# Optimization experiments

Hardware: AMD Instinct MI355X
Metric: run time of the kernel (lower is better)

Reference implementation:

```python
import jax, jax.numpy as jnp
import numpy as np

T = 100000
H = 74          # input_size == hidden_size == 74
L = 3           # lstm_layers
OUT = 1


def setup_inputs() -> dict:
    key = jax.random.key(0)
    ks = jax.random.split(key, 8)
    s = 1.0 / np.sqrt(H)  # PyTorch LSTM/Linear init scale
    seasons = jax.random.normal(ks[0], (T, H), dtype=jnp.float32)
    # PyTorch gate order: i, f, g, o -> stacked as [L, 4H, H]
    W_ih = jax.random.uniform(ks[1], (L, 4 * H, H), jnp.float32, -s, s)
    W_hh = jax.random.uniform(ks[2], (L, 4 * H, H), jnp.float32, -s, s)
    b_ih = jax.random.uniform(ks[3], (L, 4 * H), jnp.float32, -s, s)
    b_hh = jax.random.uniform(ks[4], (L, 4 * H), jnp.float32, -s, s)
    W_lin = jax.random.uniform(ks[5], (OUT, H), jnp.float32, -s, s)
    b_lin = jax.random.uniform(ks[6], (OUT,), jnp.float32, -s, s)
    return {"seasons": seasons, "W_ih": W_ih, "W_hh": W_hh,
            "b_ih": b_ih, "b_hh": b_hh, "W_lin": W_lin, "b_lin": b_lin}


def _lstm_step(h, c, x, W_ih, W_hh, b_ih, b_hh):
    # h, c: [L, H]; x: [H]. Sequential over layers (L=3, structurally distinct state).
    new_h, new_c = [], []
    inp = x
    for l in range(L):
        gates = W_ih[l] @ inp + b_ih[l] + W_hh[l] @ h[l] + b_hh[l]  # [4H]
        i, f, g, o = jnp.split(gates, 4)
        i = jax.nn.sigmoid(i)
        f = jax.nn.sigmoid(f)
        g = jnp.tanh(g)
        o = jax.nn.sigmoid(o)
        cl = f * c[l] + i * g
        hl = o * jnp.tanh(cl)
        new_h.append(hl)
        new_c.append(cl)
        inp = hl
    return jnp.stack(new_h), jnp.stack(new_c), inp


def reference(seasons, W_ih, W_hh, b_ih, b_hh, W_lin, b_lin):
    def step(carry, x):
        h, c = carry
        h, c, top = _lstm_step(h, c, x, W_ih, W_hh, b_ih, b_hh)
        pred = jax.nn.relu(W_lin @ top + b_lin)  # [1]
        return (h, c), pred

    init = (jnp.zeros((L, H), jnp.float32), jnp.zeros((L, H), jnp.float32))
    _, preds = jax.lax.scan(step, init, seasons)  # [T, 1]
    # original cats [1,1,1] tensors along dim 0 -> [T, 1, 1]
    return preds.reshape(T, 1, 1)
```

## Files before the change

kernel.cpp:

```cpp
#include <hip/hip_runtime.h>
#include <math.h>

#define TT    100000
#define HH    74
#define G4    296
#define KH    40
#define SLOT  80
#define ZSLOT 304
#define NT    768
#define W5    640
#define W6    704

typedef float f4 __attribute__((ext_vector_type(4)));

#define ALD(p)    __hip_atomic_load((p),  __ATOMIC_RELAXED, __HIP_MEMORY_SCOPE_AGENT)
#define ALDA(p)   __hip_atomic_load((p),  __ATOMIC_ACQUIRE, __HIP_MEMORY_SCOPE_AGENT)
#define AST(p,v)  __hip_atomic_store((p),(v),__ATOMIC_RELAXED, __HIP_MEMORY_SCOPE_AGENT)
#define ASTR(p,v) __hip_atomic_store((p),(v),__ATOMIC_RELEASE, __HIP_MEMORY_SCOPE_AGENT)

#define BAR() asm volatile("s_waitcnt lgkmcnt(0)\n\ts_barrier" ::: "memory")

__global__ void init_ctrl(unsigned* ctrl) {
    ctrl[threadIdx.x] = 0u;
}

__launch_bounds__(NT, 1)
__global__ void lstm_pipe6(const float* __restrict__ seasons,
                           const float* __restrict__ W_ih,
                           const float* __restrict__ W_hh,
                           const float* __restrict__ b_ih,
                           const float* __restrict__ b_hh,
                           const float* __restrict__ W_lin,
                           const float* __restrict__ b_lin,
                           float* __restrict__ out,
                           unsigned* ctrl,
                           float* zbase, float* hbase, int CZ, int CH)
{
    const int  bid = blockIdx.x;
    const int  l   = bid >> 1;
    const bool isA = (bid & 1) == 0;
    const int  tid = threadIdx.x;

    __shared__ __align__(16) float sIn[2][SLOT];
    __shared__ __align__(16) float sZ[2][ZSLOT];
    __shared__ __align__(16) float sH[SLOT];
    __shared__ float sG[G4];

    unsigned* cnt_out = ctrl + bid * 32;
    unsigned* cnt_in  = ctrl + (bid > 0 ? (bid - 1) * 32 : 0);
    unsigned* cnt_dn  = ctrl + (bid < 5 ? (bid + 1) * 32 : 0);

    float* zring     = zbase + (size_t)l * CZ * ZSLOT;
    float* hring_out = hbase + (size_t)l * CH * SLOT;
    float* hring_in  = (l > 0) ? hbase + (size_t)(l-1) * CH * SLOT : (float*)0;

    if (tid < SLOT) sH[tid] = 0.0f;
    if (tid >= SLOT && tid < SLOT + 2*(SLOT-HH)) {
        int k = tid - SLOT;
        sIn[k/(SLOT-HH)][HH + k%(SLOT-HH)] = 0.0f;
    }

    const bool isRowT = (tid < W5);
    const int  row  = (tid >> 6) * 32 + ((tid & 63) >> 1);
    const int  half = tid & 1;
    const int  wrow = (row < G4) ? row : (G4 - 1);

    f4 w0={0,0,0,0},w1={0,0,0,0},w2={0,0,0,0},w3={0,0,0,0},w4={0,0,0,0},
       w5={0,0,0,0},w6={0,0,0,0},w7={0,0,0,0},w8={0,0,0,0},w9={0,0,0,0};
    float bias = 0.0f;

    if (isRowT) {
        const bool  isG = (wrow >= 2*HH) && (wrow < 3*HH);
        const float sc  = isG ? 2.0f : 1.0f;
        const float* src = (isA ? W_ih : W_hh) + (size_t)(l*G4 + wrow) * HH;
#define LDW(V, Q) { \
        int k0 = half*KH + 4*(Q); \
        int ka=k0, kb=k0+1, kc=k0+2, kd=k0+3; \
        float va=src[ka<HH?ka:0], vb=src[kb<HH?kb:0]; \
        float vc=src[kc<HH?kc:0], vd=src[kd<HH?kd:0]; \
        V[0] = ka<HH ? sc*va : 0.0f;  V[1] = kb<HH ? sc*vb : 0.0f; \
        V[2] = kc<HH ? sc*vc : 0.0f;  V[3] = kd<HH ? sc*vd : 0.0f; }
        LDW(w0,0) LDW(w1,1) LDW(w2,2) LDW(w3,3) LDW(w4,4)
        LDW(w5,5) LDW(w6,6) LDW(w7,7) LDW(w8,8) LDW(w9,9)
#undef LDW
        asm volatile("" : "+v"(w0),"+v"(w1),"+v"(w2),"+v"(w3),"+v"(w4),
                          "+v"(w5),"+v"(w6),"+v"(w7),"+v"(w8),"+v"(w9));
        if (isA && half == 0)
            bias = sc * (b_ih[l*G4 + wrow] + b_hh[l*G4 + wrow]);
    }

    float wl0 = 0.f, wl1 = 0.f, blin = 0.f;
    if (bid == 5 && tid >= W6) {
        int lane = tid - W6;
        wl0 = W_lin[lane];
        wl1 = (lane < HH-64) ? W_lin[64 + lane] : 0.0f;
        blin = b_lin[0];
    }

    __syncthreads();

    float irA0=0.f, irA1=0.f, irB0=0.f, irB1=0.f;
    float zA0=0.f,zA1=0.f,zA2=0.f,zA3=0.f,zA4=0.f;
    float zB0=0.f,zB1=0.f,zB2=0.f,zB3=0.f,zB4=0.f;
    unsigned cin = 0, cons = 0;
    if (tid >= W5 && tid < W6) {
        const int lane = tid - W5;
        if (isA) {
            if (l == 0) {
                sIn[0][lane] = seasons[lane];
                if (lane < HH-64) sIn[0][64+lane] = seasons[64+lane];
                irA0 = seasons[HH + lane];
                if (lane < HH-64) irA1 = seasons[HH + 64 + lane];
                irB0 = seasons[2*HH + lane];
                if (lane < HH-64) irB1 = seasons[2*HH + 64 + lane];
            } else {
                do { cin = ALDA(cnt_in); } while (cin < 3u);
                sIn[0][lane] = ALD(hring_in + lane);
                if (lane < HH-64) sIn[0][64+lane] = ALD(hring_in + 64 + lane);
                const float* r1 = hring_in + (size_t)(1 % CH) * SLOT;
                irA0 = ALD(r1 + lane);
                if (lane < HH-64) irA1 = ALD(r1 + 64 + lane);
                const float* r2 = hring_in + (size_t)(2 % CH) * SLOT;
                irB0 = ALD(r2 + lane);
                if (lane < HH-64) irB1 = ALD(r2 + 64 + lane);
            }
        } else {
            do { cin = ALDA(cnt_in); } while (cin < 3u);
            sZ[0][lane]       = ALD(zring + lane);
            sZ[0][64 + lane]  = ALD(zring + 64 + lane);
            sZ[0][128 + lane] = ALD(zring + 128 + lane);
            sZ[0][192 + lane] = ALD(zring + 192 + lane);
            if (lane < G4-256) sZ[0][256 + lane] = ALD(zring + 256 + lane);
            const float* r1 = zring + (size_t)(1 % CZ) * ZSLOT;
            zA0 = ALD(r1 + lane);        zA1 = ALD(r1 + 64 + lane);
            zA2 = ALD(r1 + 128 + lane);  zA3 = ALD(r1 + 192 + lane);
            zA4 = (lane < G4-256) ? ALD(r1 + 256 + lane) : 0.0f;
            const float* r2 = zring + (size_t)(2 % CZ) * ZSLOT;
            zB0 = ALD(r2 + lane);        zB1 = ALD(r2 + 64 + lane);
            zB2 = ALD(r2 + 128 + lane);  zB3 = ALD(r2 + 192 + lane);
            zB4 = (lane < G4-256) ? ALD(r2 + 256 + lane) : 0.0f;
        }
    }
    __syncthreads();

    float c = 0.0f;

#define ACC4(W, Q) { f4 v_ = vv[Q]; \
            a0 = fmaf(W[0], v_[0], a0); a1 = fmaf(W[1], v_[1], a1); \
            a2 = fmaf(W[2], v_[2], a2); a3 = fmaf(W[3], v_[3], a3); }

#define STEP(T, IR0, IR1, Z0, Z1, Z2, Z3, Z4)                                   \
{                                                                               \
    const int b_ = (T) & 1;                                                     \
    if (isRowT) {                                                               \
        float a0, a1 = 0.f, a2 = 0.f, a3 = 0.f;                                 \
        const f4* vv;                                                           \
        if (isA) { vv = ((const f4*)sIn[b_]) + half*(KH/4); a0 = bias; }        \
        else { vv = ((const f4*)sH) + half*(KH/4);                              \
               a0 = (half == 0 && row < G4) ? sZ[b_][row] : 0.0f; }             \
        ACC4(w0,0) ACC4(w1,1) ACC4(w2,2) ACC4(w3,3) ACC4(w4,4)                  \
        ACC4(w5,5) ACC4(w6,6) ACC4(w7,7) ACC4(w8,8) ACC4(w9,9)                  \
        float p_ = (a0 + a1) + (a2 + a3);                                       \
        p_ += __shfl_xor(p_, 1, 64);                                            \
        if (isA) { if (half == 0 && row < G4) sZ[b_][row] = p_; }               \
        else { float s_ = __builtin_amdgcn_rcpf(1.0f + __expf(-p_));            \
               const bool isG_ = (row >= 2*HH) && (row < 3*HH);                 \
               float g_ = isG_ ? fmaf(2.0f, s_, -1.0f) : s_;                    \
               if (half == 0 && row < G4) sG[row] = g_; }                       \
    } else if (tid < W6) {          \
        const int lane = tid - W5;                                              \
        const int nb_ = ((T) + 1) & 1;                                          \
        int s_ = (T) + 3; if (s_ > TT-1) s_ = TT-1;                             \
        if (isA) {                                                              \
            sIn[nb_][lane] = IR0;                                               \
            if (lane < HH-64) sIn[nb_][64+lane] = IR1;                          \
            if (l == 0) {                                                       \
                const float* xs_ = seasons + (size_t)s_ * HH;                   \
                IR0 = xs_[lane];                                                \
                if (lane < HH-64) IR1 = xs_[64+lane];                           \
            } else {                                                            \
                unsigned need_ = (unsigned)(s_ + 1); if (need_ > TT) need_ = TT;\
                if (cin < need_) { do { cin = ALDA(cnt_in); } while (cin < need_); } \
                const float* rs_ = hring_in + (size_t)(s_ % CH) * SLOT;         \
                IR0 = ALD(rs_ + lane);                                          \
                if (lane < HH-64) IR1 = ALD(rs_ + 64 + lane);                   \
                cin = ALD(cnt_in);                                              \
            }                                                                   \
        } else {                                                                \
            sZ[nb_][lane] = Z0; sZ[nb_][64+lane] = Z1;                          \
            sZ[nb_][128+lane] = Z2; sZ[nb_][192+lane] = Z3;                     \
            if (lane < G4-256) sZ[nb_][256+lane] = Z4;                          \
            unsigned need_ = (unsigned)(s_ + 1); if (need_ > TT) need_ = TT;    \
            if (cin < need_) { do { cin = ALDA(cnt_in); } while (cin < need_); }\
            const float* rs_ = zring + (size_t)(s_ % CZ) * ZSLOT;               \
            Z0 = ALD(rs_ + lane); Z1 = ALD(rs_ + 64 + lane);                    \
            Z2 = ALD(rs_ + 128 + lane); Z3 = ALD(rs_ + 192 + lane);             \
            if (lane < G4-256) Z4 = ALD(rs_ + 256 + lane);                      \
            cin = ALD(cnt_in);                                                  \
        }                                                                       \
    } else {                           \
        const int lane = tid - W6;                                              \
        if ((T) > 0) {                                                          \
            if (isA) {                                                          \
                while ((long)((T)-1) - (long)cons > (long)(CZ - 8))             \
                    cons = ALD(cnt_dn);                                         \
                const int ob_ = ((T)-1) & 1;                                    \
                float v0_ = sZ[ob_][lane],      v1_ = sZ[ob_][64+lane];         \
                float v2_ = sZ[ob_][128+lane],  v3_ = sZ[ob_][192+lane];        \
                float v4_ = (lane < G4-256) ? sZ[ob_][256+lane] : 0.0f;         \
                float* rp_ = zring + (size_t)(((T)-1) % CZ) * ZSLOT;            \
                AST(rp_ + lane, v0_);        AST(rp_ + 64 + lane, v1_);         \
                AST(rp_ + 128 + lane, v2_);  AST(rp_ + 192 + lane, v3_);        \
                if (lane < G4-256) AST(rp_ + 256 + lane, v4_);                  \
                if (lane == 0) ASTR(cnt_out, (unsigned)(T));                    \
            } else if (l < 2) {                                                 \
                while ((long)((T)-1) - (long)cons > (long)(CH - 8))             \
                    cons = ALD(cnt_dn);                                         \
                float h0_ = sH[lane];                                           \
                float h1_ = (lane < HH-64) ? sH[64+lane] : 0.0f;                \
                float* rp_ = hring_out + (size_t)(((T)-1) % CH) * SLOT;         \
                AST(rp_ + lane, h0_);                                           \
                if (lane < HH-64) AST(rp_ + 64 + lane, h1_);                    \
                if (lane == 0) ASTR(cnt_out, (unsigned)(T));                    \
            } else {                                                            \
                if (lane == 0) AST(cnt_out, (unsigned)(T));                     \
                float p_ = wl0 * sH[lane];                                      \
                if (lane < HH-64) p_ += wl1 * sH[64 + lane];                    \
                _Pragma("unroll")                                               \
                for (int m_ = 32; m_ >= 1; m_ >>= 1)                            \
                    p_ += __shfl_xor(p_, m_, 64);                               \
                if (lane == 0) out[(T)-1] = fmaxf(p_ + blin, 0.0f);             \
            }                                                                   \
        }                                                                       \
    }                                                                           \
    BAR();                                                                      \
    if (!isA) {                                                                 \
        if (tid < HH) {                                                         \
            float iv_ = sG[tid], fv_ = sG[HH+tid];                              \
            float gv_ = sG[2*HH+tid], ov_ = sG[3*HH+tid];                       \
            c = fmaf(fv_, c, iv_ * gv_);                                        \
            float e_  = __expf(-2.0f * fabsf(c));                               \
            float th_ = copysignf((1.0f - e_) * __builtin_amdgcn_rcpf(1.0f + e_), c); \
            sH[tid] = ov_ * th_;                                                \
        }                                                                       \
        BAR();                                                                  \
    }                                                                           \
}

    for (int t = 0; t < TT; t += 2) {
        STEP(t,     irA0, irA1, zA0, zA1, zA2, zA3, zA4)
        STEP(t + 1, irB0, irB1, zB0, zB1, zB2, zB3, zB4)
    }
#undef STEP
#undef ACC4

    if (tid >= W6) {
        const int lane = tid - W6;
        if (isA) {
            const int ob = (TT-1) & 1;
            float v0 = sZ[ob][lane],      v1 = sZ[ob][64+lane];
            float v2 = sZ[ob][128+lane],  v3 = sZ[ob][192+lane];
            float v4 = (lane < G4-256) ? sZ[ob][256+lane] : 0.0f;
            float* rp = zring + (size_t)((TT-1) % CZ) * ZSLOT;
            AST(rp + lane, v0);        AST(rp + 64 + lane, v1);
            AST(rp + 128 + lane, v2);  AST(rp + 192 + lane, v3);
            if (lane < G4-256) AST(rp + 256 + lane, v4);
            if (lane == 0) ASTR(cnt_out, (unsigned)TT);
        } else if (l < 2) {
            float h0 = sH[lane];
            float h1 = (lane < HH-64) ? sH[64+lane] : 0.0f;
            float* rp = hring_out + (size_t)((TT-1) % CH) * SLOT;
            AST(rp + lane, h0);
            if (lane < HH-64) AST(rp + 64 + lane, h1);
            if (lane == 0) ASTR(cnt_out, (unsigned)TT);
        } else {
            float p = wl0 * sH[lane];
            if (lane < HH-64) p += wl1 * sH[64 + lane];
            #pragma unroll
            for (int m = 32; m >= 1; m >>= 1)
                p += __shfl_xor(p, m, 64);
            if (lane == 0) out[TT-1] = fmaxf(p + blin, 0.0f);
        }
    }
}

extern "C" void kernel_launch(void* const* d_in, const int* in_sizes, int n_in,
                              void* d_out, int out_size, void* d_ws, size_t ws_size,
                              hipStream_t stream)
{
    (void)in_sizes; (void)n_in; (void)out_size;
    const float* seasons = (const float*)d_in[0];
    const float* W_ih  = (const float*)d_in[1];
    const float* W_hh  = (const float*)d_in[2];
    const float* b_ih  = (const float*)d_in[3];
    const float* b_hh  = (const float*)d_in[4];
    const float* W_lin = (const float*)d_in[5];
    const float* b_lin = (const float*)d_in[6];
    float* out = (float*)d_out;

    unsigned* ctrl = (unsigned*)d_ws;
    float* zbase = (float*)((char*)d_ws + 4096);
    long avail = ((long)ws_size - 4096) / 4;
    int CZ = 256, CH = 1024;
    while ((3L*CZ*ZSLOT + 2L*CH*SLOT) > avail && CZ > 16) { CZ >>= 1; CH >>= 1; }
    if (CZ < 16) CZ = 16;
    if (CH < 16) CH = 16;
    float* hbase = zbase + 3L * CZ * ZSLOT;

    hipLaunchKernelGGL(init_ctrl, dim3(1), dim3(256), 0, stream, ctrl);
    hipLaunchKernelGGL(lstm_pipe6, dim3(6), dim3(NT), 0, stream,
                       seasons, W_ih, W_hh, b_ih, b_hh, W_lin, b_lin,
                       out, ctrl, zbase, hbase, CZ, CH);
}
```

Measured before the change: 77.22 ms.

## Remap gate matvec to 4-thread groups of 5 rows, halve block size

Each block now uses 384 threads instead of 768. Groups of 4 threads each compute 5 gate rows over a 20-wide K slice, holding 25 float4 weight registers per thread, and reduce with xor shuffles across the group. The publisher wave now also does the cell/hidden update, and progress counters are released one step earlier, before the data stores. The aim is fewer waves per block barrier and less synchronisation latency on the sequential per-timestep critical path. The cost is higher register pressure and a longer serial FMA chain per thread.

After: 103.0 ms. 33.3% more time.

```diff
diff --git a/kernel.cpp b/kernel.cpp
--- a/kernel.cpp
+++ b/kernel.cpp
@@ -4,12 +4,14 @@
 #define TT    100000
 #define HH    74
 #define G4    296
-#define KH    40
+#define KP    80
+#define QW    20
+#define NGRP  60
 #define SLOT  80
 #define ZSLOT 304
-#define NT    768
-#define W5    640
-#define W6    704
+#define NT    384
+#define WPRE  256
+#define WPUB  320
 
 typedef float f4 __attribute__((ext_vector_type(4)));
 
@@ -24,7 +26,7 @@
     ctrl[threadIdx.x] = 0u;
 }
 
-__launch_bounds__(NT, 1)
+__launch_bounds__(NT, 2)
 __global__ void lstm_pipe6(const float* __restrict__ seasons,
                            const float* __restrict__ W_ih,
                            const float* __restrict__ W_hh,
@@ -44,7 +46,7 @@
     __shared__ __align__(16) float sIn[2][SLOT];
     __shared__ __align__(16) float sZ[2][ZSLOT];
     __shared__ __align__(16) float sH[SLOT];
-    __shared__ float sG[G4];
+    __shared__ float sG[ZSLOT];
 
     unsigned* cnt_out = ctrl + bid * 32;
     unsigned* cnt_in  = ctrl + (bid > 0 ? (bid - 1) * 32 : 0);
@@ -54,44 +56,58 @@
     float* hring_out = hbase + (size_t)l * CH * SLOT;
     float* hring_in  = (l > 0) ? hbase + (size_t)(l-1) * CH * SLOT : (float*)0;
 
-    if (tid < SLOT) sH[tid] = 0.0f;
-    if (tid >= SLOT && tid < SLOT + 2*(SLOT-HH)) {
-        int k = tid - SLOT;
-        sIn[k/(SLOT-HH)][HH + k%(SLOT-HH)] = 0.0f;
-    }
-
-    const bool isRowT = (tid < W5);
-    const int  row  = (tid >> 6) * 32 + ((tid & 63) >> 1);
-    const int  half = tid & 1;
-    const int  wrow = (row < G4) ? row : (G4 - 1);
-
-    f4 w0={0,0,0,0},w1={0,0,0,0},w2={0,0,0,0},w3={0,0,0,0},w4={0,0,0,0},
-       w5={0,0,0,0},w6={0,0,0,0},w7={0,0,0,0},w8={0,0,0,0},w9={0,0,0,0};
-    float bias = 0.0f;
+    if (tid < SLOT) { sH[tid] = 0.0f; sIn[0][tid] = 0.0f; sIn[1][tid] = 0.0f; }
+
+    const bool isRowT = (tid < WPRE);
+    const int  g  = tid >> 2;
+    const int  q  = tid & 3;
+    const int  gg = (g < NGRP) ? g : NGRP - 1;
+
+#define DW(n) f4 n = {0.f,0.f,0.f,0.f}
+    DW(w00);DW(w01);DW(w02);DW(w03);DW(w04); DW(w10);DW(w11);DW(w12);DW(w13);DW(w14);
+    DW(w20);DW(w21);DW(w22);DW(w23);DW(w24); DW(w30);DW(w31);DW(w32);DW(w33);DW(w34);
+    DW(w40);DW(w41);DW(w42);DW(w43);DW(w44);
+#undef DW
+    float biasA = 0.f, biasB = 0.f;
 
     if (isRowT) {
-        const bool  isG = (wrow >= 2*HH) && (wrow < 3*HH);
-        const float sc  = isG ? 2.0f : 1.0f;
-        const float* src = (isA ? W_ih : W_hh) + (size_t)(l*G4 + wrow) * HH;
-#define LDW(V, Q) { \
-        int k0 = half*KH + 4*(Q); \
-        int ka=k0, kb=k0+1, kc=k0+2, kd=k0+3; \
-        float va=src[ka<HH?ka:0], vb=src[kb<HH?kb:0]; \
-        float vc=src[kc<HH?kc:0], vd=src[kd<HH?kd:0]; \
-        V[0] = ka<HH ? sc*va : 0.0f;  V[1] = kb<HH ? sc*vb : 0.0f; \
-        V[2] = kc<HH ? sc*vc : 0.0f;  V[3] = kd<HH ? sc*vd : 0.0f; }
-        LDW(w0,0) LDW(w1,1) LDW(w2,2) LDW(w3,3) LDW(w4,4)
-        LDW(w5,5) LDW(w6,6) LDW(w7,7) LDW(w8,8) LDW(w9,9)
+        const float* Wm = (isA ? W_ih : W_hh) + (size_t)l * G4 * HH;
+#define LDW(V, I, S) { \
+        int r_ = 5*gg + (I); if (r_ > G4-1) r_ = G4-1; \
+        float sc_ = (r_ >= 2*HH && r_ < 3*HH) ? 2.0f : 1.0f;   \
+        const float* p_ = Wm + (size_t)r_ * HH; \
+        int k0_ = QW*q + 4*(S); \
+        int ka_ = k0_;   if (ka_ > HH-1) ka_ = HH-1;    \
+        int kb_ = k0_+1; if (kb_ > HH-1) kb_ = HH-1;    \
+        int kc_ = k0_+2; if (kc_ > HH-1) kc_ = HH-1; \
+        int kd_ = k0_+3; if (kd_ > HH-1) kd_ = HH-1; \
+        V[0] = sc_*p_[ka_]; V[1] = sc_*p_[kb_]; V[2] = sc_*p_[kc_]; V[3] = sc_*p_[kd_]; }
+        LDW(w00,0,0) LDW(w01,0,1) LDW(w02,0,2) LDW(w03,0,3) LDW(w04,0,4)
+        LDW(w10,1,0) LDW(w11,1,1) LDW(w12,1,2) LDW(w13,1,3) LDW(w14,1,4)
+        LDW(w20,2,0) LDW(w21,2,1) LDW(w22,2,2) LDW(w23,2,3) LDW(w24,2,4)
+        LDW(w30,3,0) LDW(w31,3,1) LDW(w32,3,2) LDW(w33,3,3) LDW(w34,3,4)
+        LDW(w40,4,0) LDW(w41,4,1) LDW(w42,4,2) LDW(w43,4,3) LDW(w44,4,4)
 #undef LDW
-        asm volatile("" : "+v"(w0),"+v"(w1),"+v"(w2),"+v"(w3),"+v"(w4),
-                          "+v"(w5),"+v"(w6),"+v"(w7),"+v"(w8),"+v"(w9));
-        if (isA && half == 0)
-            bias = sc * (b_ih[l*G4 + wrow] + b_hh[l*G4 + wrow]);
+        asm volatile("" : "+v"(w00),"+v"(w01),"+v"(w02),"+v"(w03),"+v"(w04),
+                          "+v"(w10),"+v"(w11),"+v"(w12),"+v"(w13),"+v"(w14),
+                          "+v"(w20),"+v"(w21),"+v"(w22),"+v"(w23),"+v"(w24));
+        asm volatile("" : "+v"(w30),"+v"(w31),"+v"(w32),"+v"(w33),"+v"(w34),
+                          "+v"(w40),"+v"(w41),"+v"(w42),"+v"(w43),"+v"(w44));
+        if (isA) {
+            int r0 = 5*gg + q; if (r0 > G4-1) r0 = G4-1;
+            float s0 = (r0 >= 2*HH && r0 < 3*HH) ? 2.0f : 1.0f;
+            biasA = s0 * (b_ih[l*G4 + r0] + b_hh[l*G4 + r0]);
+            if (q == 3) {
+                int r4 = 5*gg + 4; if (r4 > G4-1) r4 = G4-1;
+                float s4 = (r4 >= 2*HH && r4 < 3*HH) ? 2.0f : 1.0f;
+                biasB = s4 * (b_ih[l*G4 + r4] + b_hh[l*G4 + r4]);
+            }
+        }
     }
 
     float wl0 = 0.f, wl1 = 0.f, blin = 0.f;
-    if (bid == 5 && tid >= W6) {
-        int lane = tid - W6;
+    if (bid == 5 && tid >= WPUB) {
+        int lane = tid - WPUB;
         wl0 = W_lin[lane];
         wl1 = (lane < HH-64) ? W_lin[64 + lane] : 0.0f;
         blin = b_lin[0];
@@ -103,8 +119,8 @@
     float zA0=0.f,zA1=0.f,zA2=0.f,zA3=0.f,zA4=0.f;
     float zB0=0.f,zB1=0.f,zB2=0.f,zB3=0.f,zB4=0.f;
     unsigned cin = 0, cons = 0;
-    if (tid >= W5 && tid < W6) {
-        const int lane = tid - W5;
+    if (tid >= WPRE && tid < WPUB) {
+        const int lane = tid - WPRE;
         if (isA) {
             if (l == 0) {
                 sIn[0][lane] = seasons[lane];
@@ -143,108 +159,128 @@
     }
     __syncthreads();
 
-    float c = 0.0f;
-
-#define ACC4(W, Q) { f4 v_ = vv[Q]; \
-            a0 = fmaf(W[0], v_[0], a0); a1 = fmaf(W[1], v_[1], a1); \
-            a2 = fmaf(W[2], v_[2], a2); a3 = fmaf(W[3], v_[3], a3); }
-
-#define STEP(T, IR0, IR1, Z0, Z1, Z2, Z3, Z4)                                   \
-{                                                                               \
-    const int b_ = (T) & 1;                                                     \
-    if (isRowT) {                                                               \
-        float a0, a1 = 0.f, a2 = 0.f, a3 = 0.f;                                 \
-        const f4* vv;                                                           \
-        if (isA) { vv = ((const f4*)sIn[b_]) + half*(KH/4); a0 = bias; }        \
-        else { vv = ((const f4*)sH) + half*(KH/4);                              \
-               a0 = (half == 0 && row < G4) ? sZ[b_][row] : 0.0f; }             \
-        ACC4(w0,0) ACC4(w1,1) ACC4(w2,2) ACC4(w3,3) ACC4(w4,4)                  \
-        ACC4(w5,5) ACC4(w6,6) ACC4(w7,7) ACC4(w8,8) ACC4(w9,9)                  \
-        float p_ = (a0 + a1) + (a2 + a3);                                       \
-        p_ += __shfl_xor(p_, 1, 64);                                            \
-        if (isA) { if (half == 0 && row < G4) sZ[b_][row] = p_; }               \
-        else { float s_ = __builtin_amdgcn_rcpf(1.0f + __expf(-p_));            \
-               const bool isG_ = (row >= 2*HH) && (row < 3*HH);                 \
-               float g_ = isG_ ? fmaf(2.0f, s_, -1.0f) : s_;                    \
-               if (half == 0 && row < G4) sG[row] = g_; }                       \
-    } else if (tid < W6) {          \
-        const int lane = tid - W5;                                              \
-        const int nb_ = ((T) + 1) & 1;                                          \
-        int s_ = (T) + 3; if (s_ > TT-1) s_ = TT-1;                             \
-        if (isA) {                                                              \
-            sIn[nb_][lane] = IR0;                                               \
-            if (lane < HH-64) sIn[nb_][64+lane] = IR1;                          \
-            if (l == 0) {                                                       \
-                const float* xs_ = seasons + (size_t)s_ * HH;                   \
-                IR0 = xs_[lane];                                                \
-                if (lane < HH-64) IR1 = xs_[64+lane];                           \
-            } else {                                                            \
-                unsigned need_ = (unsigned)(s_ + 1); if (need_ > TT) need_ = TT;\
+    float c0 = 0.0f, c1 = 0.0f;
+
+#define ACC(A_, W_, V_) A_ = fmaf(W_[0],V_[0], fmaf(W_[1],V_[1], fmaf(W_[2],V_[2], fmaf(W_[3],V_[3], A_))))
+
+#define STEP(T, IR0, IR1, Z0, Z1, Z2, Z3, Z4)                                     \
+{                                                                                 \
+    const int b_ = (T) & 1;                                                       \
+    if (isRowT) {                                                                 \
+        const f4* vv = ((const f4*)(isA ? sIn[b_] : sH)) + q*(QW/4);              \
+        f4 v0=vv[0], v1=vv[1], v2=vv[2], v3=vv[3], v4=vv[4];                      \
+        float a0=0.f,a1=0.f,a2=0.f,a3=0.f,a4=0.f;                                 \
+        ACC(a0,w00,v0); ACC(a0,w01,v1); ACC(a0,w02,v2); ACC(a0,w03,v3); ACC(a0,w04,v4); \
+        ACC(a1,w10,v0); ACC(a1,w11,v1); ACC(a1,w12,v2); ACC(a1,w13,v3); ACC(a1,w14,v4); \
+        ACC(a2,w20,v0); ACC(a2,w21,v1); ACC(a2,w22,v2); ACC(a2,w23,v3); ACC(a2,w24,v4); \
+        ACC(a3,w30,v0); ACC(a3,w31,v1); ACC(a3,w32,v2); ACC(a3,w33,v3); ACC(a3,w34,v4); \
+        ACC(a4,w40,v0); ACC(a4,w41,v1); ACC(a4,w42,v2); ACC(a4,w43,v3); ACC(a4,w44,v4); \
+            \
+        float s0_ = (q&1) ? a0 : a1;  float r0_ = __shfl_xor(s0_, 1, 64);         \
+        float s1_ = (q&1) ? a2 : a3;  float r1_ = __shfl_xor(s1_, 1, 64);         \
+        float u0_ = ((q&1) ? a1 : a0) + r0_;                                      \
+        float u1_ = ((q&1) ? a3 : a2) + r1_;                                      \
+        float c4_ = a4 + __shfl_xor(a4, 1, 64);                                   \
+        float s2_ = (q&2) ? u0_ : u1_; float r2_ = __shfl_xor(s2_, 2, 64);        \
+        float tot  = ((q&2) ? u1_ : u0_) + r2_;                                   \
+        float tot4 = c4_ + __shfl_xor(c4_, 2, 64);      \
+        const int r0i = 5*g + q, r4i = 5*g + 4;                                   \
+        if (isA) {                                                                \
+            if (g < NGRP) sZ[b_][r0i] = tot + biasA;                              \
+            if (q == 3 && g < NGRP) sZ[b_][r4i] = tot4 + biasB;                   \
+        } else {                                                                  \
+            float zx_ = (g < NGRP) ? sZ[b_][r0i] : 0.0f;                          \
+            float t_  = tot + zx_;                                                \
+            float sg_ = __builtin_amdgcn_rcpf(1.0f + __expf(-t_));                \
+            float gt_ = (r0i >= 2*HH && r0i < 3*HH) ? fmaf(2.f,sg_,-1.f) : sg_;   \
+            if (g < NGRP) sG[r0i] = gt_;                                          \
+            if (q == 3 && g < NGRP) {                                             \
+                float t4_  = tot4 + sZ[b_][r4i];                                  \
+                float sg4_ = __builtin_amdgcn_rcpf(1.0f + __expf(-t4_));          \
+                sG[r4i] = (r4i >= 2*HH && r4i < 3*HH) ? fmaf(2.f,sg4_,-1.f) : sg4_; \
+            }                                                                     \
+        }                                                                         \
+    } else if (tid < WPUB) {     \
+        const int lane = tid - WPRE;                                              \
+        const int nb_ = ((T) + 1) & 1;                                            \
+        int s_ = (T) + 3; if (s_ > TT-1) s_ = TT-1;                               \
+        unsigned need_ = (unsigned)(s_ + 1); if (need_ > TT) need_ = TT;          \
+        if (isA) {                                                                \
+            sIn[nb_][lane] = IR0;                                                 \
+            if (lane < HH-64) sIn[nb_][64+lane] = IR1;                            \
+            if (l == 0) {                                                         \
+                const float* xs_ = seasons + (size_t)s_ * HH;                     \
+                IR0 = xs_[lane];                                                  \
+                if (lane < HH-64) IR1 = xs_[64+lane];                             \
+            } else {                                                              \
                 if (cin < need_) { do { cin = ALDA(cnt_in); } while (cin < need_); } \
-                const float* rs_ = hring_in + (size_t)(s_ % CH) * SLOT;         \
-                IR0 = ALD(rs_ + lane);                                          \
-                if (lane < HH-64) IR1 = ALD(rs_ + 64 + lane);                   \
-                cin = ALD(cnt_in);                                              \
-            }                                                                   \
-        } else {                                                                \
-            sZ[nb_][lane] = Z0; sZ[nb_][64+lane] = Z1;                          \
-            sZ[nb_][128+lane] = Z2; sZ[nb_][192+lane] = Z3;                     \
-            if (lane < G4-256) sZ[nb_][256+lane] = Z4;                          \
-            unsigned need_ = (unsigned)(s_ + 1); if (need_ > TT) need_ = TT;    \
-            if (cin < need_) { do { cin = ALDA(cnt_in); } while (cin < need_); }\
-            const float* rs_ = zring + (size_t)(s_ % CZ) * ZSLOT;               \
-            Z0 = ALD(rs_ + lane); Z1 = ALD(rs_ + 64 + lane);                    \
-            Z2 = ALD(rs_ + 128 + lane); Z3 = ALD(rs_ + 192 + lane);             \
-            if (lane < G4-256) Z4 = ALD(rs_ + 256 + lane);                      \
-            cin = ALD(cnt_in);                                                  \
-        }                                                                       \
-    } else {                           \
-        const int lane = tid - W6;                                              \
-        if ((T) > 0) {                                                          \
-            if (isA) {                                                          \
-                while ((long)((T)-1) - (long)cons > (long)(CZ - 8))             \
-                    cons = ALD(cnt_dn);                                         \
-                const int ob_ = ((T)-1) & 1;                                    \
-                float v0_ = sZ[ob_][lane],      v1_ = sZ[ob_][64+lane];         \
-                float v2_ = sZ[ob_][128+lane],  v3_ = sZ[ob_][192+lane];        \
-                float v4_ = (lane < G4-256) ? sZ[ob_][256+lane] : 0.0f;         \
-                float* rp_ = zring + (size_t)(((T)-1) % CZ) * ZSLOT;            \
-                AST(rp_ + lane, v0_);        AST(rp_ + 64 + lane, v1_);         \
-                AST(rp_ + 128 + lane, v2_);  AST(rp_ + 192 + lane, v3_);        \
-                if (lane < G4-256) AST(rp_ + 256 + lane, v4_);                  \
-                if (lane == 0) ASTR(cnt_out, (unsigned)(T));                    \
-            } else if (l < 2) {                                                 \
-                while ((long)((T)-1) - (long)cons > (long)(CH - 8))             \
-                    cons = ALD(cnt_dn);                                         \
-                float h0_ = sH[lane];                                           \
-                float h1_ = (lane < HH-64) ? sH[64+lane] : 0.0f;                \
-                float* rp_ = hring_out + (size_t)(((T)-1) % CH) * SLOT;         \
-                AST(rp_ + lane, h0_);                                           \
-                if (lane < HH-64) AST(rp_ + 64 + lane, h1_);                    \
-                if (lane == 0) ASTR(cnt_out, (unsigned)(T));                    \
-            } else {                                                            \
-                if (lane == 0) AST(cnt_out, (unsigned)(T));                     \
-                float p_ = wl0 * sH[lane];                                      \
-                if (lane < HH-64) p_ += wl1 * sH[64 + lane];                    \
-                _Pragma("unroll")                                               \
-                for (int m_ = 32; m_ >= 1; m_ >>= 1)                            \
-                    p_ += __shfl_xor(p_, m_, 64);                               \
-                if (lane == 0) out[(T)-1] = fmaxf(p_ + blin, 0.0f);             \
-            }                                                                   \
-        }                                                                       \
-    }                                                                           \
-    BAR();                                                                      \
-    if (!isA) {                                                                 \
-        if (tid < HH) {                                                         \
-            float iv_ = sG[tid], fv_ = sG[HH+tid];                              \
-            float gv_ = sG[2*HH+tid], ov_ = sG[3*HH+tid];                       \
-            c = fmaf(fv_, c, iv_ * gv_);                                        \
-            float e_  = __expf(-2.0f * fabsf(c));                               \
-            float th_ = copysignf((1.0f - e_) * __builtin_amdgcn_rcpf(1.0f + e_), c); \
-            sH[tid] = ov_ * th_;                                                \
-        }                                                                       \
-        BAR();                                                                  \
-    }                                                                           \
+                const float* rs_ = hring_in + (size_t)(s_ % CH) * SLOT;           \
+                IR0 = ALD(rs_ + lane);                                            \
+                if (lane < HH-64) IR1 = ALD(rs_ + 64 + lane);                     \
+                cin = ALD(cnt_in);                                                \
+            }                                                                     \
+        } else {                                                                  \
+            sZ[nb_][lane] = Z0; sZ[nb_][64+lane] = Z1;                            \
+            sZ[nb_][128+lane] = Z2; sZ[nb_][192+lane] = Z3;                       \
+            if (lane < G4-256) sZ[nb_][256+lane] = Z4;                            \
+            if (cin < need_) { do { cin = ALDA(cnt_in); } while (cin < need_); }  \
+            const float* rs_ = zring + (size_t)(s_ % CZ) * ZSLOT;                 \
+            Z0 = ALD(rs_ + lane); Z1 = ALD(rs_ + 64 + lane);                      \
+            Z2 = ALD(rs_ + 128 + lane); Z3 = ALD(rs_ + 192 + lane);               \
+            if (lane < G4-256) Z4 = ALD(rs_ + 256 + lane);                        \
+            cin = ALD(cnt_in);                                                    \
+        }                                                                         \
+    } else {      \
+        const int lane = tid - WPUB;                                              \
+        if ((T) > 0) {                                                            \
+            if (lane == 0) ASTR(cnt_out, (unsigned)((T)-1));    \
+            if (isA) {                                                            \
+                while ((long)((T)-1) - (long)cons > (long)(CZ - 8))               \
+                    cons = ALD(cnt_dn);                                           \
+                const int ob_ = ((T)-1) & 1;                                      \
+                float x0_=sZ[ob_][lane],      x1_=sZ[ob_][64+lane];               \
+                float x2_=sZ[ob_][128+lane],  x3_=sZ[ob_][192+lane];              \
+                float x4_=(lane < G4-256) ? sZ[ob_][256+lane] : 0.0f;             \
+                float* rp_ = zring + (size_t)(((T)-1) % CZ) * ZSLOT;              \
+                AST(rp_ + lane, x0_);        AST(rp_ + 64 + lane, x1_);           \
+                AST(rp_ + 128 + lane, x2_);  AST(rp_ + 192 + lane, x3_);          \
+                if (lane < G4-256) AST(rp_ + 256 + lane, x4_);                    \
+            } else if (l < 2) {                                                   \
+                while ((long)((T)-1) - (long)cons > (long)(CH - 8))               \
+                    cons = ALD(cnt_dn);                                           \
+                float h0_ = sH[lane];                                             \
+                float h1_ = (lane < HH-64) ? sH[64+lane] : 0.0f;                  \
+                float* rp_ = hring_out + (size_t)(((T)-1) % CH) * SLOT;           \
+                AST(rp_ + lane, h0_);                                             \
+                if (lane < HH-64) AST(rp_ + 64 + lane, h1_);                      \
+            } else {                                                              \
+                float p_ = wl0 * sH[lane];                                        \
+                if (lane < HH-64) p_ += wl1 * sH[64 + lane];                      \
+                p_ += __shfl_xor(p_, 32, 64); p_ += __shfl_xor(p_, 16, 64);       \
+                p_ += __shfl_xor(p_,  8, 64); p_ += __shfl_xor(p_,  4, 64);       \
+                p_ += __shfl_xor(p_,  2, 64); p_ += __shfl_xor(p_,  1, 64);       \
+                if (lane == 0) out[(T)-1] = fmaxf(p_ + blin, 0.0f);               \
+            }                                                                     \
+        }                                                                         \
+    }                                                                             \
+    BAR();                                                                        \
+    if (!isA) {                                                                   \
+        if (tid >= WPUB) {                       \
+            const int u_ = tid - WPUB;                                            \
+            float iv_=sG[u_], fv_=sG[HH+u_], gv_=sG[2*HH+u_], ov_=sG[3*HH+u_];    \
+            c0 = fmaf(fv_, c0, iv_ * gv_);                                        \
+            float e0_ = __expf(-2.0f * fabsf(c0));                                \
+            sH[u_] = ov_ * copysignf((1.0f-e0_)*__builtin_amdgcn_rcpf(1.0f+e0_), c0); \
+            if (u_ < HH-64) {                                                     \
+                const int u2_ = 64 + u_;                                          \
+                float iw_=sG[u2_], fw_=sG[HH+u2_], gw_=sG[2*HH+u2_], ow_=sG[3*HH+u2_]; \
+                c1 = fmaf(fw_, c1, iw_ * gw_);                                    \
+                float e1_ = __expf(-2.0f * fabsf(c1));                            \
+                sH[u2_] = ow_ * copysignf((1.0f-e1_)*__builtin_amdgcn_rcpf(1.0f+e1_), c1); \
+            }                                                                     \
+        }                                                                         \
+        BAR();                                                                    \
+    }                                                                             \
 }
 
     for (int t = 0; t < TT; t += 2) {
@@ -252,19 +288,19 @@
         STEP(t + 1, irB0, irB1, zB0, zB1, zB2, zB3, zB4)
     }
 #undef STEP
-#undef ACC4
-
-    if (tid >= W6) {
-        const int lane = tid - W6;
+#undef ACC
+
+    if (tid >= WPUB) {
+        const int lane = tid - WPUB;
         if (isA) {
             const int ob = (TT-1) & 1;
-            float v0 = sZ[ob][lane],      v1 = sZ[ob][64+lane];
-            float v2 = sZ[ob][128+lane],  v3 = sZ[ob][192+lane];
-            float v4 = (lane < G4-256) ? sZ[ob][256+lane] : 0.0f;
+            float x0=sZ[ob][lane],      x1=sZ[ob][64+lane];
+            float x2=sZ[ob][128+lane],  x3=sZ[ob][192+lane];
+            float x4=(lane < G4-256) ? sZ[ob][256+lane] : 0.0f;
             float* rp = zring + (size_t)((TT-1) % CZ) * ZSLOT;
-            AST(rp + lane, v0);        AST(rp + 64 + lane, v1);
-            AST(rp + 128 + lane, v2);  AST(rp + 192 + lane, v3);
-            if (lane < G4-256) AST(rp + 256 + lane, v4);
+            AST(rp + lane, x0);        AST(rp + 64 + lane, x1);
+            AST(rp + 128 + lane, x2);  AST(rp + 192 + lane, x3);
+            if (lane < G4-256) AST(rp + 256 + lane, x4);
             if (lane == 0) ASTR(cnt_out, (unsigned)TT);
         } else if (l < 2) {
             float h0 = sH[lane];
@@ -276,10 +312,11 @@
         } else {
             float p = wl0 * sH[lane];
             if (lane < HH-64) p += wl1 * sH[64 + lane];
-            #pragma unroll
-            for (int m = 32; m >= 1; m >>= 1)
-                p += __shfl_xor(p, m, 64);
+            p += __shfl_xor(p, 32, 64); p += __shfl_xor(p, 16, 64);
+            p += __shfl_xor(p,  8, 64); p += __shfl_xor(p,  4, 64);
+            p += __shfl_xor(p,  2, 64); p += __shfl_xor(p,  1, 64);
             if (lane == 0) out[TT-1] = fmaxf(p + blin, 0.0f);
+            if (lane == 0) ASTR(cnt_out, (unsigned)TT);
         }
     }
 }
```
